# Kernel optimization log

Hardware: AMD Instinct MI355X
Metric: run time of the kernel (lower is better)

## Reference

```python
import jax, jax.numpy as jnp
import numpy as np

B, T, D_IN = 4, 512, 4096
H, G, HD = 32, 8, 128            # num_heads, num_kv_groups, head_dim
GS = H // G                      # group_size
CACHE = 3584                     # prev cache length (uniform across batch)
S = CACHE + T                    # total kv length
ROPE_BASE = 10000.0


def _rope_tables(max_pos, head_dim):
    inv_freq = 1.0 / (ROPE_BASE ** (jnp.arange(0, head_dim, 2, dtype=jnp.float32) / head_dim))
    angles = jnp.arange(max_pos, dtype=jnp.float32)[:, None] * inv_freq[None, :]  # [S, hd/2]
    angles = jnp.concatenate([angles, angles], axis=-1)                            # [S, hd]
    return jnp.cos(angles), jnp.sin(angles)


def apply_rope(x, cos, sin, start_positions):
    # x: [B, nH, T, hd]; cos/sin: [S, hd]; start_positions: [B] int
    t = x.shape[2]
    pos = start_positions[:, None] + jnp.arange(t)       # [B, T]
    c = cos[pos][:, None, :, :]                          # [B, 1, T, hd]
    s = sin[pos][:, None, :, :]
    x1, x2 = jnp.split(x, 2, axis=-1)
    rotated = jnp.concatenate([-x2, x1], axis=-1)
    return x * c + rotated * s


def setup_inputs() -> dict:
    key = jax.random.key(0)
    ks = jax.random.split(key, 8)
    x = jax.random.normal(ks[0], (B, T, D_IN), dtype=jnp.float32)
    cos, sin = _rope_tables(S, HD)
    start_positions = jnp.full((B,), CACHE, dtype=jnp.int32)
    # causal mask over absolute positions: query i sits at CACHE+i; True = masked
    kv_pos = jnp.arange(S)[None, None, None, :]
    q_pos = (CACHE + jnp.arange(T))[None, None, :, None]
    mask = jnp.broadcast_to(kv_pos > q_pos, (B, 1, T, S))
    prev_k = jax.random.normal(ks[1], (B, G, CACHE, HD), dtype=jnp.float32)
    prev_v = jax.random.normal(ks[2], (B, G, CACHE, HD), dtype=jnp.float32)
    sc = 0.02
    q_w = jax.random.normal(ks[3], (D_IN, H * HD), dtype=jnp.float32) * sc
    k_w = jax.random.normal(ks[4], (D_IN, G * HD), dtype=jnp.float32) * sc
    v_w = jax.random.normal(ks[5], (D_IN, G * HD), dtype=jnp.float32) * sc
    o_w = jax.random.normal(ks[6], (H * HD, H * HD), dtype=jnp.float32) * sc
    return {"x": x, "mask": mask, "cos": cos, "sin": sin,
            "start_positions": start_positions, "prev_k": prev_k, "prev_v": prev_v,
            "q_w": q_w, "k_w": k_w, "v_w": v_w, "o_w": o_w}


def reference(x, mask, cos, sin, start_positions, prev_k, prev_v, q_w, k_w, v_w, o_w):
    b, t, _ = x.shape
    q = (x @ q_w).reshape(b, t, H, HD).transpose(0, 2, 1, 3)   # [B,H,T,hd]
    k = (x @ k_w).reshape(b, t, G, HD).transpose(0, 2, 1, 3)   # [B,G,T,hd]
    v = (x @ v_w).reshape(b, t, G, HD).transpose(0, 2, 1, 3)   # [B,G,T,hd]
    q = apply_rope(q, cos, sin, start_positions)
    k = apply_rope(k, cos, sin, start_positions)
    # cache concat (uniform lengths -> padded batch concat)
    k_all = jnp.concatenate([prev_k, k], axis=2)               # [B,G,S,hd]
    v_all = jnp.concatenate([prev_v, v], axis=2)
    # GQA expansion: repeat each kv group for its group of query heads
    k_rep = jnp.repeat(k_all, GS, axis=1)                      # [B,H,S,hd]
    v_rep = jnp.repeat(v_all, GS, axis=1)
    scores = jnp.einsum('bhtd,bhsd->bhts', q, k_rep)
    scores = jnp.where(mask, -jnp.inf, scores)
    attn = jax.nn.softmax(scores / jnp.sqrt(jnp.asarray(HD, x.dtype)), axis=-1)
    ctx = jnp.einsum('bhts,bhsd->bthd', attn, v_rep).reshape(b, t, H * HD)
    out = ctx @ o_w
    return out, k_all, v_all
```

## Files before the change

kernel.cpp:

```cpp
#include <hip/hip_runtime.h>

#define B_     4
#define T_     512
#define DIN    4096
#define H_     32
#define G_     8
#define HD_    128
#define S_     4096
#define CACHE_ 3584
#define M_     2048
#define NQKV   6144
#define SCALE  0.08838834764831843f
#define LOG2E  1.4426950408889634f
#define QSC    (SCALE * LOG2E)

typedef __attribute__((ext_vector_type(4)))  float  f32x4;
typedef __attribute__((ext_vector_type(16))) float  f32x16;
typedef __attribute__((ext_vector_type(8)))  short  s16x8;
typedef __attribute__((ext_vector_type(4)))  unsigned short u16x4;
typedef __attribute__((ext_vector_type(8)))  unsigned short u16x8;
typedef __attribute__((ext_vector_type(4)))  unsigned int   u32x4;
typedef unsigned short u16;
typedef unsigned int   u32;

__device__ __forceinline__ u16 f2bf(float f) {
  u32 u = __builtin_bit_cast(u32, f);
  return (u16)((u + 0x7fffu + ((u >> 16) & 1u)) >> 16);
}
__device__ __forceinline__ float bf2f(u16 h) {
  return __builtin_bit_cast(float, (u32)h << 16);
}
__device__ __forceinline__ f32x4 mfma16(s16x8 a, s16x8 b, f32x4 c) {
  return __builtin_amdgcn_mfma_f32_16x16x32_bf16(a, b, c, 0, 0, 0);
}
__device__ __forceinline__ u32 pkbf(float a, float b) {
  u32 r; asm("v_cvt_pk_bf16_f32 %0, %1, %2" : "=v"(r) : "v"(a), "v"(b)); return r;
}
__device__ __forceinline__ void gload_lds16(const void* g, void* l) {
  __builtin_amdgcn_global_load_lds((__attribute__((address_space(1))) void*)g,
                                   (__attribute__((address_space(3))) void*)l, 16, 0, 0);
}

__global__ __launch_bounds__(256) void k_cvt_x(const float* __restrict__ x, u16* __restrict__ xb) {
  size_t i = ((size_t)blockIdx.x * 256 + threadIdx.x) * 4;
  f32x4 v = *(const f32x4*)(x + i);
  u16x4 o = { f2bf(v[0]), f2bf(v[1]), f2bf(v[2]), f2bf(v[3]) };
  *(u16x4*)(xb + i) = o;
}

__global__ __launch_bounds__(256) void k_twt(const float* __restrict__ src, int ldn,
                                             u16* __restrict__ dst) {
  __shared__ float tile[64][68];
  int k0 = blockIdx.x * 64, n0 = blockIdx.y * 64;
  int t = threadIdx.x;
  int rr = t >> 4, cc = (t & 15) * 4;
#pragma unroll
  for (int p = 0; p < 4; ++p) {
    int r = p * 16 + rr;
    f32x4 v = *(const f32x4*)(src + (size_t)(k0 + r) * ldn + n0 + cc);
    tile[r][cc] = v[0]; tile[r][cc + 1] = v[1]; tile[r][cc + 2] = v[2]; tile[r][cc + 3] = v[3];
  }
  __syncthreads();
#pragma unroll
  for (int p = 0; p < 4; ++p) {
    int n = p * 16 + rr;
    u16x4 o = { f2bf(tile[cc][n]), f2bf(tile[cc + 1][n]), f2bf(tile[cc + 2][n]), f2bf(tile[cc + 3][n]) };
    *(u16x4*)(dst + (size_t)(n0 + n) * 4096 + k0 + cc) = o;
  }
}

__global__ __launch_bounds__(256) void k_prep_k(const float* __restrict__ pk,
                                                float* __restrict__ k_all, u16* __restrict__ kb) {
  int bg = blockIdx.y;
  size_t si = ((size_t)blockIdx.x * 256 + threadIdx.x) * 4;
  f32x4 v = *(const f32x4*)(pk + (size_t)bg * CACHE_ * HD_ + si);
  size_t dof = (size_t)bg * S_ * HD_ + si;
  *(f32x4*)(k_all + dof) = v;
  u16x4 o = { f2bf(v[0]), f2bf(v[1]), f2bf(v[2]), f2bf(v[3]) };
  *(u16x4*)(kb + dof) = o;
}

__global__ __launch_bounds__(256) void k_prep_v(const float* __restrict__ pv,
                                                float* __restrict__ v_all, u16* __restrict__ vt) {
  __shared__ float tile[64][132];
  int bg = blockIdx.y, s0 = blockIdx.x * 64;
  int t = threadIdx.x;
  const float* src = pv + ((size_t)bg * CACHE_ + s0) * HD_;
  float* dc = v_all + ((size_t)bg * S_ + s0) * HD_;
  int r8 = t >> 5, c4 = (t & 31) * 4;
#pragma unroll
  for (int p = 0; p < 8; ++p) {
    int r = p * 8 + r8;
    f32x4 v = *(const f32x4*)(src + (size_t)r * HD_ + c4);
    *(f32x4*)(dc + (size_t)r * HD_ + c4) = v;
    tile[r][c4] = v[0]; tile[r][c4 + 1] = v[1]; tile[r][c4 + 2] = v[2]; tile[r][c4 + 3] = v[3];
  }
  __syncthreads();
  int hr = t >> 4, s4 = (t & 15) * 4;
#pragma unroll
  for (int p = 0; p < 8; ++p) {
    int hd = p * 16 + hr;
    u16x4 o = { f2bf(tile[s4][hd]), f2bf(tile[s4 + 1][hd]), f2bf(tile[s4 + 2][hd]), f2bf(tile[s4 + 3][hd]) };
    *(u16x4*)(vt + ((size_t)bg * HD_ + hd) * S_ + s0 + s4) = o;
  }
}

template<bool OUT_F32>
__global__ __launch_bounds__(256) void k_gemm(const u16* __restrict__ A, const u16* __restrict__ Bt,
                                              void* __restrict__ Cp, int N, int K) {
  __shared__ u16 As[128 * 64];
  __shared__ u16 Bs[128 * 64];
  const int tid = threadIdx.x;
  const int m0 = blockIdx.x * 128, n0 = blockIdx.y * 128;
  const int wave = tid >> 6, lane = tid & 63;
  const int wm = (wave >> 1) * 64, wn = (wave & 1) * 64;
  const int cl = lane & 15, kl = (lane >> 4) * 8;
  const int srow = wave * 32 + (lane >> 3);
  const int scol = (lane & 7) * 8;
  f32x4 acc[4][4] = {};
  for (int k0 = 0; k0 < K; k0 += 64) {
    __syncthreads();
#pragma unroll
    for (int i = 0; i < 4; ++i) {
      gload_lds16(A  + (size_t)(m0 + srow + i * 8) * K + k0 + scol, As + (wave * 32 + i * 8) * 64);
      gload_lds16(Bt + (size_t)(n0 + srow + i * 8) * K + k0 + scol, Bs + (wave * 32 + i * 8) * 64);
    }
    __syncthreads();
#pragma unroll
    for (int kk = 0; kk < 2; ++kk) {
      s16x8 af[4], bfr[4];
#pragma unroll
      for (int mi = 0; mi < 4; ++mi) af[mi]  = *(const s16x8*)(As + (wm + mi * 16 + cl) * 64 + kk * 32 + kl);
#pragma unroll
      for (int ni = 0; ni < 4; ++ni) bfr[ni] = *(const s16x8*)(Bs + (wn + ni * 16 + cl) * 64 + kk * 32 + kl);
#pragma unroll
      for (int mi = 0; mi < 4; ++mi)
#pragma unroll
        for (int ni = 0; ni < 4; ++ni)
          acc[mi][ni] = mfma16(af[mi], bfr[ni], acc[mi][ni]);
    }
  }
  const int rl = (lane >> 4) * 4;
#pragma unroll
  for (int mi = 0; mi < 4; ++mi)
#pragma unroll
    for (int ni = 0; ni < 4; ++ni) {
      int col = n0 + wn + ni * 16 + cl;
#pragma unroll
      for (int r = 0; r < 4; ++r) {
        int rw = m0 + wm + mi * 16 + rl + r;
        if (OUT_F32) ((float*)Cp)[(size_t)rw * N + col] = acc[mi][ni][r];
        else         ((u16*)Cp)[(size_t)rw * N + col]   = f2bf(acc[mi][ni][r]);
      }
    }
}

__global__ __launch_bounds__(256) void k_rope(const u16* __restrict__ qkv, const float* __restrict__ cosT,
                                              const float* __restrict__ sinT, const int* __restrict__ sp,
                                              u16* __restrict__ qr, u16* __restrict__ kb,
                                              float* __restrict__ k_all, float* __restrict__ v_all) {
  int bt = blockIdx.x;
  int b = bt >> 9, t = bt & 511;
  int pos = sp[b] + t;
  const u16* row = qkv + (size_t)bt * NQKV;
  for (int idx = threadIdx.x; idx < 2560; idx += 256) {
    int head = idx >> 6, d = idx & 63;
    float c = cosT[pos * HD_ + d], s = sinT[pos * HD_ + d];
    float x1 = bf2f(row[head * HD_ + d]);
    float x2 = bf2f(row[head * HD_ + d + 64]);
    float y1 = x1 * c - x2 * s;
    float y2 = x2 * c + x1 * s;
    if (head < 32) {
      size_t o = (((size_t)b * H_ + head) * T_ + t) * HD_ + d;
      qr[o] = f2bf(y1 * QSC); qr[o + 64] = f2bf(y2 * QSC);
    } else {
      int g = head - 32;
      size_t o = (((size_t)b * G_ + g) * S_ + CACHE_ + t) * HD_ + d;
      kb[o] = f2bf(y1); kb[o + 64] = f2bf(y2);
      k_all[o] = y1; k_all[o + 64] = y2;
    }
  }
  for (int idx = threadIdx.x; idx < 1024; idx += 256) {
    int g = idx >> 7;
    float v = bf2f(row[5120 + idx]);
    size_t o = (((size_t)b * G_ + g) * S_ + CACHE_ + t) * HD_ + (idx & 127);
    v_all[o] = v;
  }
}

__global__ __launch_bounds__(256) void k_tv_new(const u16* __restrict__ qkv, u16* __restrict__ vt) {
  __shared__ u16 tile[64][72];
  int bg = blockIdx.y;
  int b = bg >> 3, g = bg & 7;
  int tt = blockIdx.x >> 1, ht = blockIdx.x & 1;
  int t0 = tt * 64, hd0 = ht * 64;
  int t = threadIdx.x;
  int rr = t >> 3, c8 = (t & 7) * 8;
#pragma unroll
  for (int p = 0; p < 2; ++p) {
    int r = p * 32 + rr;
    *(u16x8*)(&tile[r][c8]) =
      *(const u16x8*)(qkv + (size_t)(b * T_ + t0 + r) * NQKV + 5120 + g * HD_ + hd0 + c8);
  }
  __syncthreads();
  int hr = t >> 4, s4 = (t & 15) * 4;
#pragma unroll
  for (int p = 0; p < 4; ++p) {
    int hd = p * 16 + hr;
    u16x4 o = { tile[s4][hd], tile[s4 + 1][hd], tile[s4 + 2][hd], tile[s4 + 3][hd] };
    *(u16x4*)(vt + ((size_t)bg * HD_ + hd0 + hd) * S_ + CACHE_ + t0 + s4) = o;
  }
}

__global__ __launch_bounds__(512, 2) void k_attn(const u16* __restrict__ Q, const u16* __restrict__ Kc,
                                                 const u16* __restrict__ Vt, const int* __restrict__ sp,
                                                 u16* __restrict__ ctx) {
  __shared__ u16 Ks[64 * 128];
  __shared__ u16 Vs[128 * 64];
  const int qh = blockIdx.x, h = blockIdx.y, b = blockIdx.z;
  const int g = h >> 2;
  const int tid = threadIdx.x, w = tid >> 6, lane = tid & 63;
  const int l31 = lane & 31, hh = lane >> 5;
  const int cache = sp[b];
  const int qbase = qh * 256;
  const int qtok = qbase + w * 32 + l31;
  const size_t kvoff = (size_t)(b * G_ + g) * S_ * HD_;
  const u16* kp = Kc + kvoff;
  const u16* vp = Vt + kvoff;
  s16x8 qreg[8];
  {
    const u16* qb = Q + ((size_t)(b * H_ + h) * T_ + qtok) * HD_;
#pragma unroll
    for (int s = 0; s < 8; ++s) qreg[s] = *(const s16x8*)(qb + s * 16 + hh * 8);
  }
  f32x16 acc[4] = {};
  float mr = -1e30f, ls = 0.f;
  const int krow = w * 8 + (lane >> 3), kch = lane & 7;
  const int vrow = w * 16 + (lane >> 2), vch = lane & 3;
  const int kswz = (krow & 15) << 3;
  const int vswz = (vrow & 7) << 3;
  const int rdswzK = (l31 & 15) << 3;
  const int rdswzV = (l31 & 7) << 3;
  const int jm = (cache + qbase + w * 32) >> 6;
  const int jlastB = (cache + qbase + 255) >> 6;
  const int kvlim = cache + qtok;
  u16x8 rk0 = *(const u16x8*)(kp + (size_t)krow * HD_ + kch * 8);
  u16x8 rk1 = *(const u16x8*)(kp + (size_t)krow * HD_ + (kch + 8) * 8);
  u16x8 rv0 = *(const u16x8*)(vp + (size_t)vrow * S_ + vch * 8);
  u16x8 rv1 = *(const u16x8*)(vp + (size_t)vrow * S_ + (vch + 4) * 8);
  for (int j = 0; j <= jlastB; ++j) {
    __syncthreads();
    *(u16x8*)(Ks + krow * 128 + ((kch * 8) ^ kswz))        = rk0;
    *(u16x8*)(Ks + krow * 128 + (((kch + 8) * 8) ^ kswz))  = rk1;
    *(u16x8*)(Vs + vrow * 64 + ((vch * 8) ^ vswz))         = rv0;
    *(u16x8*)(Vs + vrow * 64 + (((vch + 4) * 8) ^ vswz))   = rv1;
    __syncthreads();
    if (j < jlastB) {
      rk0 = *(const u16x8*)(kp + (size_t)((j + 1) * 64 + krow) * HD_ + kch * 8);
      rk1 = *(const u16x8*)(kp + (size_t)((j + 1) * 64 + krow) * HD_ + (kch + 8) * 8);
      rv0 = *(const u16x8*)(vp + (size_t)vrow * S_ + (j + 1) * 64 + vch * 8);
      rv1 = *(const u16x8*)(vp + (size_t)vrow * S_ + (j + 1) * 64 + vch * 8 + 32);
    }
    f32x16 sa[2] = {};
#pragma unroll
    for (int s = 0; s < 8; ++s) {
      s16x8 ka = *(const s16x8*)(Ks + l31 * 128 + ((s * 16 + hh * 8) ^ rdswzK));
      sa[0] = __builtin_amdgcn_mfma_f32_32x32x16_bf16(ka, qreg[s], sa[0], 0, 0, 0);
    }
#pragma unroll
    for (int s = 0; s < 8; ++s) {
      s16x8 ka = *(const s16x8*)(Ks + (32 + l31) * 128 + ((s * 16 + hh * 8) ^ rdswzK));
      sa[1] = __builtin_amdgcn_mfma_f32_32x32x16_bf16(ka, qreg[s], sa[1], 0, 0, 0);
    }
    if (j >= jm) {
#pragma unroll
      for (int r = 0; r < 16; ++r) {
        int kv = j * 64 + (r & 3) + 8 * (r >> 2) + 4 * hh;
        if (kv > kvlim)      sa[0][r] = -1e30f;
        if (kv + 32 > kvlim) sa[1][r] = -1e30f;
      }
    }
    float mx = sa[0][0];
#pragma unroll
    for (int r = 1; r < 16; ++r) mx = fmaxf(mx, sa[0][r]);
#pragma unroll
    for (int r = 0; r < 16; ++r) mx = fmaxf(mx, sa[1][r]);
    mx = fmaxf(mx, __shfl_xor(mx, 32));
    if (__any(mx > mr + 8.f)) {
      float nm = fmaxf(mr, mx);
      float al = __builtin_amdgcn_exp2f(mr - nm);
      mr = nm; ls *= al;
#pragma unroll
      for (int r = 0; r < 16; ++r) {
        float ar = __shfl(al, (r & 3) + 8 * (r >> 2) + 4 * hh, 64);
        acc[0][r] *= ar; acc[1][r] *= ar; acc[2][r] *= ar; acc[3][r] *= ar;
      }
    }
    float rs = 0.f;
#pragma unroll
    for (int r = 0; r < 16; ++r) { sa[0][r] = __builtin_amdgcn_exp2f(sa[0][r] - mr); rs += sa[0][r]; }
#pragma unroll
    for (int r = 0; r < 16; ++r) { sa[1][r] = __builtin_amdgcn_exp2f(sa[1][r] - mr); rs += sa[1][r]; }
    rs += __shfl_xor(rs, 32);
    ls += rs;
    s16x8 pf[4];
#pragma unroll
    for (int sb = 0; sb < 2; ++sb) {
      u32 a0 = pkbf(sa[sb][0],  sa[sb][1]),  a1 = pkbf(sa[sb][2],  sa[sb][3]);
      u32 b0 = pkbf(sa[sb][4],  sa[sb][5]),  b1 = pkbf(sa[sb][6],  sa[sb][7]);
      u32 c0 = pkbf(sa[sb][8],  sa[sb][9]),  c1 = pkbf(sa[sb][10], sa[sb][11]);
      u32 d0 = pkbf(sa[sb][12], sa[sb][13]), d1 = pkbf(sa[sb][14], sa[sb][15]);
      u32 xa0 = __shfl_xor(a0, 32), xa1 = __shfl_xor(a1, 32);
      u32 xb0 = __shfl_xor(b0, 32), xb1 = __shfl_xor(b1, 32);
      u32 xc0 = __shfl_xor(c0, 32), xc1 = __shfl_xor(c1, 32);
      u32 xd0 = __shfl_xor(d0, 32), xd1 = __shfl_xor(d1, 32);
      u32x4 f0 = { hh ? xb0 : a0, hh ? xb1 : a1, hh ? b0 : xa0, hh ? b1 : xa1 };
      u32x4 f1 = { hh ? xd0 : c0, hh ? xd1 : c1, hh ? d0 : xc0, hh ? d1 : xc1 };
      pf[sb * 2]     = __builtin_bit_cast(s16x8, f0);
      pf[sb * 2 + 1] = __builtin_bit_cast(s16x8, f1);
    }
#pragma unroll
    for (int hb = 0; hb < 4; ++hb) {
      const int vro = hb * 32 + l31;
#pragma unroll
      for (int kb = 0; kb < 4; ++kb) {
        s16x8 vb = *(const s16x8*)(Vs + vro * 64 + ((kb * 16 + hh * 8) ^ rdswzV));
        acc[hb] = __builtin_amdgcn_mfma_f32_32x32x16_bf16(pf[kb], vb, acc[hb], 0, 0, 0);
      }
    }
  }
  float inv = 1.0f / ls;
#pragma unroll
  for (int r = 0; r < 16; ++r) {
    int ql = (r & 3) + 8 * (r >> 2) + 4 * hh;
    float ivr = __shfl(inv, ql, 64);
    u16* cb = ctx + ((size_t)(b * T_ + qbase + w * 32 + ql)) * 4096 + h * HD_ + l31;
    cb[0]  = f2bf(acc[0][r] * ivr);
    cb[32] = f2bf(acc[1][r] * ivr);
    cb[64] = f2bf(acc[2][r] * ivr);
    cb[96] = f2bf(acc[3][r] * ivr);
  }
}

extern "C" void kernel_launch(void* const* d_in, const int* in_sizes, int n_in,
                              void* d_out, int out_size, void* d_ws, size_t ws_size,
                              hipStream_t stream) {
  const float* x      = (const float*)d_in[0];
  const float* cosT   = (const float*)d_in[2];
  const float* sinT   = (const float*)d_in[3];
  const int*   sp     = (const int*)d_in[4];
  const float* prev_k = (const float*)d_in[5];
  const float* prev_v = (const float*)d_in[6];
  const float* q_w    = (const float*)d_in[7];
  const float* k_w    = (const float*)d_in[8];
  const float* v_w    = (const float*)d_in[9];
  const float* o_w    = (const float*)d_in[10];

  float* out   = (float*)d_out;
  float* k_all = out + (size_t)B_ * T_ * H_ * HD_;
  float* v_all = k_all + (size_t)B_ * G_ * S_ * HD_;

  char* w = (char*)d_ws;
  u16* wt_qkv = (u16*)(w);
  u16* wt_o   = (u16*)(w + 50331648);
  u16* x_bf   = (u16*)(w + 83886080);
  u16* qkv_bf = (u16*)(w + 100663296);
  u16* q_rope = (u16*)(w + 125829120);
  u16* k_bf   = (u16*)(w + 142606336);
  u16* v_t    = (u16*)(w + 176160768);
  u16* ctx    = (u16*)(w + 209715200);
  if (ws_size < 226492416ull) return;

  k_cvt_x<<<8192, 256, 0, stream>>>(x, x_bf);
  k_twt<<<dim3(64, 64), 256, 0, stream>>>(q_w, 4096, wt_qkv);
  k_twt<<<dim3(64, 16), 256, 0, stream>>>(k_w, 1024, wt_qkv + (size_t)4096 * 4096);
  k_twt<<<dim3(64, 16), 256, 0, stream>>>(v_w, 1024, wt_qkv + (size_t)5120 * 4096);
  k_twt<<<dim3(64, 64), 256, 0, stream>>>(o_w, 4096, wt_o);
  k_prep_k<<<dim3(448, 32), 256, 0, stream>>>(prev_k, k_all, k_bf);
  k_prep_v<<<dim3(56, 32), 256, 0, stream>>>(prev_v, v_all, v_t);
  k_gemm<false><<<dim3(16, 48), 256, 0, stream>>>(x_bf, wt_qkv, qkv_bf, NQKV, 4096);
  k_rope<<<2048, 256, 0, stream>>>(qkv_bf, cosT, sinT, sp, q_rope, k_bf, k_all, v_all);
  k_tv_new<<<dim3(16, 32), 256, 0, stream>>>(qkv_bf, v_t);
  k_attn<<<dim3(2, 32, 4), 512, 0, stream>>>(q_rope, k_bf, v_t, sp, ctx);
  k_gemm<true><<<dim3(16, 32), 256, 0, stream>>>(ctx, wt_o, out, 4096, 4096);
}
```

Baseline: 591.6 us.

## Replace GEMM with double-buffered 512-thread kernel using swizzled LDS and XCD remap

Replaces the single-buffered 128x128 GEMM with a 512-thread kernel that uses larger tiles (256x256 for QKV, 128x256 for the output projection). Global-to-LDS loads are double-buffered, with explicit vmcnt waits so the next tile's loads overlap the MFMA work. The LDS layout is XOR-swizzled to avoid bank conflicts, and workgroups are remapped across XCDs for better L2 locality. It also raises wave priority around the MFMA blocks. The risks are lower occupancy (one block per CU) and a fragile hand-tuned waitcnt schedule.

```diff
diff --git a/kernel.cpp b/kernel.cpp
--- a/kernel.cpp
+++ b/kernel.cpp
@@ -105,50 +105,95 @@
   }
 }
 
-template<bool OUT_F32>
-__global__ __launch_bounds__(256) void k_gemm(const u16* __restrict__ A, const u16* __restrict__ Bt,
-                                              void* __restrict__ Cp, int N, int K) {
-  __shared__ u16 As[128 * 64];
-  __shared__ u16 Bs[128 * 64];
-  const int tid = threadIdx.x;
-  const int m0 = blockIdx.x * 128, n0 = blockIdx.y * 128;
-  const int wave = tid >> 6, lane = tid & 63;
-  const int wm = (wave >> 1) * 64, wn = (wave & 1) * 64;
-  const int cl = lane & 15, kl = (lane >> 4) * 8;
-  const int srow = wave * 32 + (lane >> 3);
-  const int scol = (lane & 7) * 8;
-  f32x4 acc[4][4] = {};
-  for (int k0 = 0; k0 < K; k0 += 64) {
-    __syncthreads();
-#pragma unroll
-    for (int i = 0; i < 4; ++i) {
-      gload_lds16(A  + (size_t)(m0 + srow + i * 8) * K + k0 + scol, As + (wave * 32 + i * 8) * 64);
-      gload_lds16(Bt + (size_t)(n0 + srow + i * 8) * K + k0 + scol, Bs + (wave * 32 + i * 8) * 64);
-    }
-    __syncthreads();
+template<int BM, bool OUT_F32>
+__global__ __launch_bounds__(512, 1) void k_gemm2(const u16* __restrict__ A, const u16* __restrict__ Bt,
+                                                  void* __restrict__ Cp, int M, int N, int K) {
+  constexpr int MI = BM / 32;
+  constexpr int LA = BM / 64;
+  __shared__ u16 As[2 * BM * 64];
+  __shared__ u16 Bs[2 * 256 * 64];
+  const int tid = threadIdx.x, w = tid >> 6, lane = tid & 63;
+  const int wr = w >> 2, wc = w & 3;
+  const int cl = lane & 15, khi = lane >> 4;
+  const int Mt = M / BM;
+  const int nwg = gridDim.x;
+  const int q = nwg >> 3, r8 = nwg & 7;
+  const int xcd = blockIdx.x & 7, pos = blockIdx.x >> 3;
+  const int wgid = (xcd < r8 ? xcd * (q + 1) : r8 * (q + 1) + (xcd - r8) * q) + pos;
+  const int m0 = (wgid % Mt) * BM, n0 = (wgid / Mt) * 256;
+  const int rb = tid >> 3;
+  const int csw = ((tid & 7) ^ (rb & 7)) * 8;
+  const u16* aS = A  + (size_t)(m0 + rb) * K + csw;
+  const u16* bS = Bt + (size_t)(n0 + rb) * K + csw;
+  u16* aD = As + w * 512;
+  u16* bD = Bs + w * 512;
+  const int ck0 = ((0 + khi) ^ (cl & 7)) * 8;
+  const int ck1 = ((4 + khi) ^ (cl & 7)) * 8;
+  const int NT = K >> 6;
+  f32x4 acc[MI][4] = {};
+
+#define STAGE_(buf, tt)                                                                   \
+  do {                                                                                    \
+    _Pragma("unroll")                                                                     \
+    for (int i = 0; i < LA; ++i)                                                          \
+      gload_lds16(aS + (size_t)(i * 64) * K + (size_t)(tt) * 64, aD + (buf) * (BM * 64) + i * 4096); \
+    _Pragma("unroll")                                                                     \
+    for (int i = 0; i < 4; ++i)                                                           \
+      gload_lds16(bS + (size_t)(i * 64) * K + (size_t)(tt) * 64, bD + (buf) * (256 * 64) + i * 4096); \
+  } while (0)
+#define VMCNT_L_()                                                                        \
+  do {                                                                                    \
+    if constexpr (BM == 256) asm volatile("s_waitcnt vmcnt(8)" ::: "memory");             \
+    else                     asm volatile("s_waitcnt vmcnt(6)" ::: "memory");             \
+  } while (0)
+
+  STAGE_(0, 0);
+  STAGE_(1, 1);
+  VMCNT_L_();
+  __builtin_amdgcn_sched_barrier(0);
+  __builtin_amdgcn_s_barrier();
+  __builtin_amdgcn_sched_barrier(0);
+
+  for (int t = 0; t < NT; ++t) {
+    const int buf = t & 1;
+    const int ab = buf * (BM * 64) + (wr * (BM / 2) + cl) * 64;
+    const int bb = buf * (256 * 64) + (wc * 64 + cl) * 64;
 #pragma unroll
     for (int kk = 0; kk < 2; ++kk) {
-      s16x8 af[4], bfr[4];
-#pragma unroll
-      for (int mi = 0; mi < 4; ++mi) af[mi]  = *(const s16x8*)(As + (wm + mi * 16 + cl) * 64 + kk * 32 + kl);
-#pragma unroll
-      for (int ni = 0; ni < 4; ++ni) bfr[ni] = *(const s16x8*)(Bs + (wn + ni * 16 + cl) * 64 + kk * 32 + kl);
-#pragma unroll
-      for (int mi = 0; mi < 4; ++mi)
+      const int ck = kk ? ck1 : ck0;
+      s16x8 bf4[4], af[MI];
+#pragma unroll
+      for (int ni = 0; ni < 4; ++ni) bf4[ni] = *(const s16x8*)(Bs + bb + ni * 16 * 64 + ck);
+#pragma unroll
+      for (int mi = 0; mi < MI; ++mi) af[mi] = *(const s16x8*)(As + ab + mi * 16 * 64 + ck);
+      __builtin_amdgcn_s_setprio(1);
+#pragma unroll
+      for (int mi = 0; mi < MI; ++mi)
 #pragma unroll
         for (int ni = 0; ni < 4; ++ni)
-          acc[mi][ni] = mfma16(af[mi], bfr[ni], acc[mi][ni]);
-    }
-  }
-  const int rl = (lane >> 4) * 4;
-#pragma unroll
-  for (int mi = 0; mi < 4; ++mi)
+          acc[mi][ni] = mfma16(af[mi], bf4[ni], acc[mi][ni]);
+      __builtin_amdgcn_s_setprio(0);
+    }
+    __builtin_amdgcn_sched_barrier(0);
+    __builtin_amdgcn_s_barrier();
+    __builtin_amdgcn_sched_barrier(0);
+    if (t + 2 < NT) STAGE_(buf, t + 2);
+    VMCNT_L_();
+    __builtin_amdgcn_sched_barrier(0);
+    __builtin_amdgcn_s_barrier();
+    __builtin_amdgcn_sched_barrier(0);
+  }
+#undef STAGE_
+#undef VMCNT_L_
+  const int rl = khi * 4;
+#pragma unroll
+  for (int mi = 0; mi < MI; ++mi)
 #pragma unroll
     for (int ni = 0; ni < 4; ++ni) {
-      int col = n0 + wn + ni * 16 + cl;
+      int col = n0 + wc * 64 + ni * 16 + cl;
 #pragma unroll
       for (int r = 0; r < 4; ++r) {
-        int rw = m0 + wm + mi * 16 + rl + r;
+        int rw = m0 + wr * (BM / 2) + mi * 16 + rl + r;
         if (OUT_F32) ((float*)Cp)[(size_t)rw * N + col] = acc[mi][ni][r];
         else         ((u16*)Cp)[(size_t)rw * N + col]   = f2bf(acc[mi][ni][r]);
       }
@@ -378,9 +423,9 @@
   k_twt<<<dim3(64, 64), 256, 0, stream>>>(o_w, 4096, wt_o);
   k_prep_k<<<dim3(448, 32), 256, 0, stream>>>(prev_k, k_all, k_bf);
   k_prep_v<<<dim3(56, 32), 256, 0, stream>>>(prev_v, v_all, v_t);
-  k_gemm<false><<<dim3(16, 48), 256, 0, stream>>>(x_bf, wt_qkv, qkv_bf, NQKV, 4096);
+  k_gemm2<256, false><<<192, 512, 0, stream>>>(x_bf, wt_qkv, qkv_bf, M_, NQKV, 4096);
   k_rope<<<2048, 256, 0, stream>>>(qkv_bf, cosT, sinT, sp, q_rope, k_bf, k_all, v_all);
   k_tv_new<<<dim3(16, 32), 256, 0, stream>>>(qkv_bf, v_t);
   k_attn<<<dim3(2, 32, 4), 512, 0, stream>>>(q_rope, k_bf, v_t, sp, ctx);
-  k_gemm<true><<<dim3(16, 32), 256, 0, stream>>>(ctx, wt_o, out, 4096, 4096);
-}
+  k_gemm2<128, true><<<256, 512, 0, stream>>>(ctx, wt_o, out, M_, 4096, 4096);
+}
```

New measurement: 541.3 us. -8.5%, faster.
